# Kernel optimization log

Hardware: AMD Instinct MI355X
Metric: run time of the kernel (lower is better)

Reference implementation:

```python
import jax, jax.numpy as jnp
import numpy as np
from jax import lax

B, L, D, E, K, H = 8, 1024, 256, 8, 2, 1024  # batch, seq(in_channel), in_dim, experts, top_k, out_channel/hidden
LMAX = L // 2  # largest expert input dim (factor i+2 = 2)
LENS = [L // (i + 2) for i in range(E)]


def setup_inputs() -> dict:
    key = jax.random.key(0)
    ks = jax.random.split(key, 12)
    x = jax.random.normal(ks[0], (B, L, D), dtype=jnp.float32)
    conv_ws = jax.random.normal(ks[1], (3, D, D, 3), dtype=jnp.float32) / np.sqrt(3 * D)
    conv_bs = jax.random.normal(ks[2], (3, D), dtype=jnp.float32) * 0.01
    fl_w = jax.random.normal(ks[3], (E, L), dtype=jnp.float32) / np.sqrt(L)
    fl_b = jax.random.normal(ks[4], (E,), dtype=jnp.float32) * 0.01
    # expert first-layer weights, zero-padded on input axis to LMAX (expert i uses L//(i+2) inputs)
    w1 = jax.random.normal(ks[5], (E, H, LMAX), dtype=jnp.float32) / np.sqrt(LMAX)
    col_mask = (np.arange(LMAX)[None, :] < np.array(LENS)[:, None]).astype(np.float32)  # [E, LMAX]
    w1 = w1 * jnp.asarray(col_mask)[:, None, :]
    b1 = jax.random.normal(ks[6], (E, H), dtype=jnp.float32) * 0.01
    w2 = jax.random.normal(ks[7], (E, H, H), dtype=jnp.float32) / np.sqrt(H)
    b2 = jax.random.normal(ks[8], (E, H), dtype=jnp.float32) * 0.01
    w3 = jax.random.normal(ks[9], (E, H, H), dtype=jnp.float32) / np.sqrt(H)
    b3 = jax.random.normal(ks[10], (E, H), dtype=jnp.float32) * 0.01
    return {"x": x, "conv_ws": conv_ws, "conv_bs": conv_bs, "fl_w": fl_w, "fl_b": fl_b,
            "w1": w1, "b1": b1, "w2": w2, "b2": b2, "w3": w3, "b3": b3}


def _gelu(v):
    return jax.nn.gelu(v, approximate=False)  # torch nn.GELU default is exact erf


def _forward(x, conv_ws, conv_bs, fl_w, fl_b, w1, b1, w2, b2, w3, b3):
    xt = jnp.transpose(x, (0, 2, 1))  # [B, D, L]
    # --- Router: 3 dilated causal-padded ('same') convs + GELU ---
    h = xt
    for i in range(3):
        d = 2 ** i
        h = lax.conv_general_dilated(h, conv_ws[i], window_strides=(1,), padding=[(d, d)],
                                     rhs_dilation=(d,), dimension_numbers=("NCH", "OIH", "NCH"))
        h = _gelu(h + conv_bs[i][None, :, None])
    logits = jax.nn.sigmoid(jnp.einsum("bdl,el->bde", h, fl_w) + fl_b)  # [B, D, E]
    prob = jax.nn.softmax(logits, axis=-1)
    top_val, top_idx = lax.top_k(prob, K)  # [B, D, K]
    top_val = top_val / jnp.sum(top_val, axis=-1, keepdims=True)
    # combine gate per expert: gates[b,d,e] = sum_k top_val * 1[top_idx==e]
    gates = jnp.sum(top_val[..., None] * jax.nn.one_hot(top_idx, E, dtype=top_val.dtype), axis=2)  # [B, D, E]
    # --- Per-expert downsample (avg_pool1d, kernel=stride=i+2), zero-padded to LMAX ---
    xs = []
    for i in range(E):
        f = i + 2
        Li = LENS[i]
        xd = xt[:, :, :Li * f].reshape(B, D, Li, f).mean(-1)  # [B, D, Li]
        xs.append(jnp.pad(xd, ((0, 0), (0, 0), (0, LMAX - Li))))
    xe = jnp.stack(xs)  # [E, B, D, LMAX]; pad cols align with zeroed w1 cols
    # --- Expert MLPs (dense compute, masked by gates; zero gate == token not routed) ---
    h1 = _gelu(jnp.einsum("ebdl,ehl->ebdh", xe, w1) + b1[:, None, None, :])
    h2 = _gelu(jnp.einsum("ebdh,egh->ebdg", h1, w2) + b2[:, None, None, :])
    h3 = jnp.einsum("ebdg,eog->ebdo", h2, w3) + b3[:, None, None, :]  # [E, B, D, H]
    out = jnp.einsum("ebdo,bde->bdo", h3, gates)  # scatter-add combine, [B, D, H]
    return jnp.transpose(out, (0, 2, 1))  # [B, L(out_channel), D]


def reference(x, conv_ws, conv_bs, fl_w, fl_b, w1, b1, w2, b2, w3, b3):
    return _forward(x, conv_ws, conv_bs, fl_w, fl_b, w1, b1, w2, b2, w3, b3)
```

## Files before the change

kernel.cpp:

```cpp
#include <hip/hip_runtime.h>
#include <math.h>

#define Bb 8
#define Ll 1024
#define Dd 256
#define Ee 8
#define Hh 1024
#define LMAXc 512
#define NTOK (Bb*Dd)
#define LPAD 1032
#define MAXTILES 72

typedef short bf16x8 __attribute__((ext_vector_type(8)));
typedef float f32x4 __attribute__((ext_vector_type(4)));
typedef unsigned short u16x8 __attribute__((ext_vector_type(8)));

__device__ __forceinline__ float gelu_f(float x) {
    return 0.5f * x * (1.0f + erff(x * 0.70710678118654752440f));
}
__device__ __forceinline__ unsigned short f2b(float x) {
    unsigned int u = __float_as_uint(x);
    return (unsigned short)((u + 0x7fffu + ((u >> 16) & 1u)) >> 16);
}
__device__ __forceinline__ float b2f(unsigned short h) {
    return __uint_as_float(((unsigned int)h) << 16);
}
__device__ __forceinline__ void gl_lds16(const void* g, void* l) {
    __builtin_amdgcn_global_load_lds((const __attribute__((address_space(1))) unsigned int*)g,
                                     (__attribute__((address_space(3))) unsigned int*)l, 16, 0, 0);
}

__global__ __launch_bounds__(256) void prep_all(
    const float* __restrict__ x, const float* __restrict__ cw,
    unsigned short* __restrict__ xhi, unsigned short* __restrict__ xlo,
    unsigned short* __restrict__ chi, unsigned short* __restrict__ clo,
    unsigned short* __restrict__ wchi, unsigned short* __restrict__ wclo,
    unsigned short* __restrict__ xe)
{
    int blk = blockIdx.x;
    int t = threadIdx.x;
    if (blk < 4096) {
        int u = blk;
        int e = u >> 9;
        int b = (u >> 6) & 7;
        int c = u & 63;
        int f = e + 2;
        int Li = Ll / f;
        int j0 = c * 8;
        if (j0 >= Li) return;
        int d = t;
        float invf = 1.0f / (float)f;
        int lim = Li - 1;
        float v[8] = {};
        for (int r = 0; r < f; ++r) {
            #pragma unroll
            for (int jj = 0; jj < 8; ++jj) {
                int j = j0 + jj; if (j > lim) j = lim;
                v[jj] += x[((size_t)(b * Ll + j * f + r)) * Dd + d];
            }
        }
        size_t obase = ((size_t)(e * NTOK + b * 256 + d)) * LMAXc + j0;
        if (j0 + 8 <= Li) {
            u16x8 hv;
            #pragma unroll
            for (int q = 0; q < 8; ++q) hv[q] = (short)f2b(v[q] * invf);
            *(u16x8*)(xe + obase) = hv;
        } else {
            for (int jj = 0; jj < Li - j0; ++jj)
                xe[obase + jj] = f2b(v[jj] * invf);
        }
    } else if (blk < 4128) {
        int u = (blk - 4096) * 256 + t;
        int f = u >> 11;
        int rem = u & 2047;
        int b = rem >> 8;
        int r2 = rem & 255;
        int row = r2 >> 5;
        int col = (r2 & 31) * 8;
        int padrow = (row < 4) ? row : (1024 + row);
        unsigned short* buf = (f == 0) ? xhi : (f == 1) ? xlo : (f == 2) ? chi : clo;
        u16x8 z = {0, 0, 0, 0, 0, 0, 0, 0};
        *(u16x8*)(buf + (size_t)(b * LPAD + padrow) * Dd + col) = z;
    } else if (blk < 4384) {
        int cb = blk - 4128;
        const float4* s4 = (const float4*)x;
        size_t ob = (size_t)cb * 1024 + t;
        float4 v[8];
        #pragma unroll
        for (int it = 0; it < 4; ++it) {
            v[2 * it]     = s4[(ob + it * 256) * 2];
            v[2 * it + 1] = s4[(ob + it * 256) * 2 + 1];
        }
        #pragma unroll
        for (int it = 0; it < 4; ++it) {
            size_t o = ob + it * 256;
            int d8 = (int)(o & 31), l = (int)((o >> 5) & 1023), b = (int)(o >> 15);
            size_t ooff = (size_t)(b * LPAD + 4 + l) * Dd + d8 * 8;
            float vv[8] = {v[2*it].x, v[2*it].y, v[2*it].z, v[2*it].w,
                           v[2*it+1].x, v[2*it+1].y, v[2*it+1].z, v[2*it+1].w};
            u16x8 hv, lv;
            #pragma unroll
            for (int q = 0; q < 8; ++q) {
                unsigned short h = f2b(vv[q]);
                hv[q] = (short)h;
                lv[q] = (short)f2b(vv[q] - b2f(h));
            }
            *(u16x8*)(xhi + ooff) = hv;
            *(u16x8*)(xlo + ooff) = lv;
        }
    } else {
        int cb = blk - 4384;
        int idx0 = (cb * 256 + t) * 8;
        float vv[8];
        #pragma unroll
        for (int q = 0; q < 8; ++q) {
            int idx = idx0 + q;
            int i = idx & (Dd - 1);
            int o = (idx >> 8) & (Dd - 1);
            int lk = idx >> 16;
            int layer = lk / 3;
            int k = lk % 3;
            vv[q] = cw[(((size_t)layer * Dd + o) * Dd + i) * 3 + k];
        }
        u16x8 hv, lv;
        #pragma unroll
        for (int q = 0; q < 8; ++q) {
            unsigned short h = f2b(vv[q]);
            hv[q] = (short)h;
            lv[q] = (short)f2b(vv[q] - b2f(h));
        }
        *(u16x8*)(wchi + idx0) = hv;
        *(u16x8*)(wclo + idx0) = lv;
    }
}

template<int MODE, int CVT>
__global__ __launch_bounds__(256, 2) void conv_mfma(
    const unsigned short* __restrict__ inhi, const unsigned short* __restrict__ inlo,
    const unsigned short* __restrict__ whiL, const unsigned short* __restrict__ wloL,
    const float* __restrict__ bias,
    unsigned short* __restrict__ outhi, unsigned short* __restrict__ outlo,
    const float* __restrict__ flw, float* __restrict__ logits,
    const float* __restrict__ cvsrc, unsigned short* __restrict__ cvd1,
    unsigned short* __restrict__ cvd2, int dil)
{
    __shared__ char smem[32768];

    if (CVT && blockIdx.y >= (Dd / 64)) {
        int cb = (blockIdx.y - Dd / 64) * 128 + blockIdx.x;
        int t = threadIdx.x;
        const float4* s4 = (const float4*)cvsrc;
        size_t ob = (size_t)cb * 1024 + t;
        float4 v[8];
        #pragma unroll
        for (int it = 0; it < 4; ++it) {
            v[2 * it]     = s4[(ob + it * 256) * 2];
            v[2 * it + 1] = s4[(ob + it * 256) * 2 + 1];
        }
        #pragma unroll
        for (int it = 0; it < 4; ++it) {
            size_t o = ob + it * 256;
            float vv[8] = {v[2*it].x, v[2*it].y, v[2*it].z, v[2*it].w,
                           v[2*it+1].x, v[2*it+1].y, v[2*it+1].z, v[2*it+1].w};
            u16x8 hv, lv;
            #pragma unroll
            for (int q = 0; q < 8; ++q) {
                unsigned short h = f2b(vv[q]);
                hv[q] = (short)h;
                if (CVT == 1) lv[q] = (short)f2b(vv[q] - b2f(h));
            }
            *(u16x8*)(cvd1 + o * 8) = hv;
            if (CVT == 1) *(u16x8*)(cvd2 + o * 8) = lv;
        }
        return;
    }

    char* sAhi = smem;
    char* sAlo = smem + 8192;
    char* sBhi = smem + 16384;
    char* sBlo = smem + 24576;

    const int t = threadIdx.x;
    const int lane = t & 63, w = t >> 6;
    const int r16 = lane & 15, quad = lane >> 4;
    const int wr = w >> 1, wc = w & 1;
    const int row0 = blockIdx.x * 64;
    const int col0 = blockIdx.y * 64;
    const int b = row0 >> 10, l0 = row0 & 1023;

    int aoff[2], boff[2];
    #pragma unroll
    for (int i = 0; i < 2; ++i) {
        int ra = wr * 32 + i * 16 + r16;
        aoff[i] = ra * 64 + ((quad ^ ((ra >> 1) & 3)) << 4);
        int rb = wc * 32 + i * 16 + r16;
        boff[i] = rb * 64 + ((quad ^ ((rb >> 1) & 3)) << 4);
    }
    const int rs = t >> 2, ce = ((t & 3) ^ ((rs >> 1) & 3)) << 3;
    const unsigned short* gAhi = inhi + (size_t)(b * LPAD + 4 + l0 + rs) * Dd + ce;
    const unsigned short* gAlo = inlo + (size_t)(b * LPAD + 4 + l0 + rs) * Dd + ce;

    f32x4 acc[2][2];
    const f32x4 zero4 = {0.f, 0.f, 0.f, 0.f};
    #pragma unroll
    for (int i = 0; i < 2; ++i)
        #pragma unroll
        for (int j = 0; j < 2; ++j) acc[i][j] = zero4;

    for (int tap = 0; tap < 3; ++tap) {
        const int sh = (tap - 1) * dil;
        const unsigned short* pAhi = gAhi + sh * Dd;
        const unsigned short* pAlo = gAlo + sh * Dd;
        const unsigned short* gBhi = whiL + ((size_t)tap * Dd + col0 + rs) * Dd + ce;
        const unsigned short* gBlo = wloL + ((size_t)tap * Dd + col0 + rs) * Dd + ce;
        for (int kb = 0; kb < Dd; kb += 64) {
            gl_lds16(pAhi + kb,      sAhi + (w << 10));
            gl_lds16(pAhi + kb + 32, sAhi + 4096 + (w << 10));
            gl_lds16(pAlo + kb,      sAlo + (w << 10));
            gl_lds16(pAlo + kb + 32, sAlo + 4096 + (w << 10));
            gl_lds16(gBhi + kb,      sBhi + (w << 10));
            gl_lds16(gBhi + kb + 32, sBhi + 4096 + (w << 10));
            gl_lds16(gBlo + kb,      sBlo + (w << 10));
            gl_lds16(gBlo + kb + 32, sBlo + 4096 + (w << 10));
            __syncthreads();
            #pragma unroll
            for (int h = 0; h < 2; ++h) {
                const int ho = h * 4096;
                bf16x8 ah[2], al[2], bh[2], bl[2];
                #pragma unroll
                for (int i = 0; i < 2; ++i) {
                    ah[i] = *(const bf16x8*)(sAhi + ho + aoff[i]);
                    al[i] = *(const bf16x8*)(sAlo + ho + aoff[i]);
                    bh[i] = *(const bf16x8*)(sBhi + ho + boff[i]);
                    bl[i] = *(const bf16x8*)(sBlo + ho + boff[i]);
                }
                #pragma unroll
                for (int mi = 0; mi < 2; ++mi)
                    #pragma unroll
                    for (int ni = 0; ni < 2; ++ni) {
                        acc[mi][ni] = __builtin_amdgcn_mfma_f32_16x16x32_bf16(ah[mi], bh[ni], acc[mi][ni], 0, 0, 0);
                        acc[mi][ni] = __builtin_amdgcn_mfma_f32_16x16x32_bf16(ah[mi], bl[ni], acc[mi][ni], 0, 0, 0);
                        acc[mi][ni] = __builtin_amdgcn_mfma_f32_16x16x32_bf16(al[mi], bh[ni], acc[mi][ni], 0, 0, 0);
                    }
            }
            __syncthreads();
        }
    }

    int cc[2]; float bv[2];
    #pragma unroll
    for (int ni = 0; ni < 2; ++ni) {
        cc[ni] = col0 + wc * 32 + ni * 16 + r16;
        bv[ni] = bias[cc[ni]];
    }
    if (MODE == 0) {
        #pragma unroll
        for (int mi = 0; mi < 2; ++mi) {
            int lb = l0 + wr * 32 + mi * 16 + quad * 4;
            #pragma unroll
            for (int reg = 0; reg < 4; ++reg) {
                int l = lb + reg;
                #pragma unroll
                for (int ni = 0; ni < 2; ++ni) {
                    float v = gelu_f(acc[mi][ni][reg] + bv[ni]);
                    size_t o = (size_t)(b * LPAD + 4 + l) * Dd + cc[ni];
                    unsigned short h = f2b(v);
                    outhi[o] = h;
                    outlo[o] = f2b(v - b2f(h));
                }
            }
        }
    } else {
        float* wl   = (float*)smem;
        float* slog = (float*)(smem + 2048);
        for (int i = t; i < 512; i += 256) {
            int ll = i >> 3, e = i & 7;
            wl[i] = flw[e * Ll + l0 + ll];
            slog[i] = 0.0f;
        }
        __syncthreads();
        float part[2][8];
        #pragma unroll
        for (int ni = 0; ni < 2; ++ni)
            #pragma unroll
            for (int e = 0; e < 8; ++e) part[ni][e] = 0.0f;
        #pragma unroll
        for (int mi = 0; mi < 2; ++mi) {
            #pragma unroll
            for (int reg = 0; reg < 4; ++reg) {
                int ll = wr * 32 + mi * 16 + quad * 4 + reg;
                #pragma unroll
                for (int ni = 0; ni < 2; ++ni) {
                    float v = gelu_f(acc[mi][ni][reg] + bv[ni]);
                    #pragma unroll
                    for (int e = 0; e < 8; ++e) part[ni][e] += v * wl[ll * 8 + e];
                }
            }
        }
        #pragma unroll
        for (int ni = 0; ni < 2; ++ni) {
            int dl = wc * 32 + ni * 16 + r16;
            #pragma unroll
            for (int e = 0; e < 8; ++e) atomicAdd(&slog[dl * 8 + e], part[ni][e]);
        }
        __syncthreads();
        for (int i = t; i < 512; i += 256) {
            int dl = i >> 3, e = i & 7;
            atomicAdd(&logits[(size_t)(b * Dd + col0 + dl) * Ee + e], slog[i]);
        }
    }
}

template<int MODE, int GATHER, int TWOPASS>
__global__ __launch_bounds__(256, 4) void gemm_sp(
    const unsigned short* __restrict__ AG,
    const unsigned short* __restrict__ BhiG, const unsigned short* __restrict__ BloG,
    const float* __restrict__ biasG, const float* __restrict__ gates,
    const int* __restrict__ cntG, const int* __restrict__ listG,
    const int* __restrict__ tileTab, const int* __restrict__ ntiles,
    unsigned short* __restrict__ Cout, float* __restrict__ outf,
    int M, int N, int K)
{
    if (blockIdx.y >= ntiles[0]) return;
    const int desc = tileTab[blockIdx.y];
    const int e = desc >> 16;
    const int row0 = (desc & 0xffff) * 64;
    const int cn = cntG[e];

    constexpr int NCH = TWOPASS ? 2 : 4;
    __shared__ char smem[TWOPASS ? 24576 : 32768];
    char* sA   = smem;
    char* sBhi = smem + NCH * 4096;
    char* sBlo = smem + 2 * NCH * 4096;

    const unsigned short* Bhi = BhiG + (size_t)e * N * K;
    const unsigned short* Blo = TWOPASS ? (BloG + (size_t)e * N * K) : nullptr;
    const float* bias = biasG + (size_t)e * N;

    int Keff = K;
    if (GATHER) {
        int Li = Ll / (e + 2);
        Keff = ((Li + 63) >> 6) << 6;
    }

    const int t = threadIdx.x;
    const int lane = t & 63, w = t >> 6;
    const int r16 = lane & 15, quad = lane >> 4;
    const int wr = w >> 1, wc = w & 1;
    const int col0 = blockIdx.x * 64;

    int aoff[2], boff[2];
    #pragma unroll
    for (int i = 0; i < 2; ++i) {
        int ra = wr * 32 + i * 16 + r16;
        aoff[i] = ra * 64 + ((quad ^ ((ra >> 1) & 3)) << 4);
        int rb = wc * 32 + i * 16 + r16;
        boff[i] = rb * 64 + ((quad ^ ((rb >> 1) & 3)) << 4);
    }
    const int r0s = t >> 2, c0s = ((t & 3) ^ ((r0s >> 1) & 3)) << 3;
    int ri = row0 + r0s; if (ri > cn - 1) ri = cn - 1;
    const int ar = GATHER ? listG[e * NTOK + ri] : ri;
    const unsigned short* gA  = AG + ((size_t)e * M + ar) * K + c0s;
    const unsigned short* gB  = Bhi + (size_t)(col0 + r0s) * K + c0s;
    const unsigned short* gBl = TWOPASS ? (Blo + (size_t)(col0 + r0s) * K + c0s) : nullptr;
    const int wofs = w << 10;

    f32x4 acc[2][2];
    const f32x4 zero4 = {0.f, 0.f, 0.f, 0.f};
    #pragma unroll
    for (int i = 0; i < 2; ++i)
        #pragma unroll
        for (int j = 0; j < 2; ++j) acc[i][j] = zero4;

    for (int k0 = 0; k0 < Keff; k0 += NCH * 32) {
        #pragma unroll
        for (int c = 0; c < NCH; ++c) {
            gl_lds16(gA + k0 + c * 32, sA + c * 4096 + wofs);
            gl_lds16(gB + k0 + c * 32, sBhi + c * 4096 + wofs);
        }
        if (TWOPASS) {
            #pragma unroll
            for (int c = 0; c < NCH; ++c)
                gl_lds16(gBl + k0 + c * 32, sBlo + c * 4096 + wofs);
        }
        __syncthreads();
        #pragma unroll
        for (int h = 0; h < NCH; ++h) {
            const int ho = h * 4096;
            bf16x8 ah[2], bh[2];
            #pragma unroll
            for (int i = 0; i < 2; ++i) {
                ah[i] = *(const bf16x8*)(sA + ho + aoff[i]);
                bh[i] = *(const bf16x8*)(sBhi + ho + boff[i]);
            }
            #pragma unroll
            for (int mi = 0; mi < 2; ++mi)
                #pragma unroll
                for (int ni = 0; ni < 2; ++ni)
                    acc[mi][ni] = __builtin_amdgcn_mfma_f32_16x16x32_bf16(ah[mi], bh[ni], acc[mi][ni], 0, 0, 0);
            if (TWOPASS) {
                bf16x8 bl[2];
                #pragma unroll
                for (int i = 0; i < 2; ++i) bl[i] = *(const bf16x8*)(sBlo + ho + boff[i]);
                #pragma unroll
                for (int mi = 0; mi < 2; ++mi)
                    #pragma unroll
                    for (int ni = 0; ni < 2; ++ni)
                        acc[mi][ni] = __builtin_amdgcn_mfma_f32_16x16x32_bf16(ah[mi], bl[ni], acc[mi][ni], 0, 0, 0);
            }
        }
        __syncthreads();
    }

    int cc[2]; float bv[2];
    #pragma unroll
    for (int ni = 0; ni < 2; ++ni) {
        cc[ni] = col0 + wc * 32 + ni * 16 + r16;
        bv[ni] = bias[cc[ni]];
    }
    if (MODE == 0) {
        unsigned short* CE = Cout + (size_t)e * M * N;
        #pragma unroll
        for (int mi = 0; mi < 2; ++mi) {
            int rb = row0 + wr * 32 + mi * 16 + quad * 4;
            #pragma unroll
            for (int reg = 0; reg < 4; ++reg) {
                size_t roff = (size_t)(rb + reg) * N;
                #pragma unroll
                for (int ni = 0; ni < 2; ++ni)
                    CE[roff + cc[ni]] = f2b(gelu_f(acc[mi][ni][reg] + bv[ni]));
            }
        }
    } else {
        #pragma unroll
        for (int mi = 0; mi < 2; ++mi) {
            int rb = row0 + wr * 32 + mi * 16 + quad * 4;
            #pragma unroll
            for (int reg = 0; reg < 4; ++reg) {
                int i = rb + reg;
                if (i < cn) {
                    int tok = listG[e * NTOK + i];
                    float g = gates[(size_t)tok * Ee + e];
                    size_t roff = ((size_t)e * NTOK + i) * N;
                    #pragma unroll
                    for (int ni = 0; ni < 2; ++ni)
                        outf[roff + cc[ni]] = g * (acc[mi][ni][reg] + bv[ni]);
                }
            }
        }
    }
}


__global__ __launch_bounds__(256) void gates_topk(const float* __restrict__ logits,
                                                  const float* __restrict__ fl_b,
                                                  float* __restrict__ gates,
                                                  int* __restrict__ cnt,
                                                  int* __restrict__ list,
                                                  int* __restrict__ rowidx) {
    const int tok = blockIdx.x * 256 + threadIdx.x;
    const int lane = threadIdx.x & 63;
    const unsigned long long ltmask = (1ull << lane) - 1ull;

    float s[Ee];
    #pragma unroll
    for (int e = 0; e < Ee; ++e) {
        float z = logits[tok * Ee + e] + fl_b[e];
        s[e] = 1.0f / (1.0f + expf(-z));
    }
    float mx = s[0];
    #pragma unroll
    for (int e = 1; e < Ee; ++e) mx = fmaxf(mx, s[e]);
    float p[Ee];
    #pragma unroll
    for (int e = 0; e < Ee; ++e) p[e] = expf(s[e] - mx);
    int i1 = 0;
    #pragma unroll
    for (int e = 1; e < Ee; ++e) if (p[e] > p[i1]) i1 = e;
    int i2 = (i1 == 0) ? 1 : 0;
    #pragma unroll
    for (int e = 0; e < Ee; ++e) {
        if (e == i1 || e == i2) continue;
        if (p[e] > p[i2]) i2 = e;
    }
    float inv = 1.0f / (p[i1] + p[i2]);
    #pragma unroll
    for (int e = 0; e < Ee; ++e) gates[tok * Ee + e] = 0.0f;
    gates[tok * Ee + i1] = p[i1] * inv;
    gates[tok * Ee + i2] = p[i2] * inv;

    #pragma unroll
    for (int slot = 0; slot < 2; ++slot) {
        int ie = slot ? i2 : i1;
        for (int e = 0; e < Ee; ++e) {
            unsigned long long m = __ballot(ie == e);
            if (m) {
                int leader = __ffsll((long long)m) - 1;
                int base = 0;
                if (lane == leader) base = atomicAdd(&cnt[e], (int)__popcll(m));
                base = __shfl(base, leader);
                if (ie == e) {
                    int pos = base + (int)__popcll(m & ltmask);
                    list[e * NTOK + pos] = tok;
                    rowidx[tok * 2 + slot] = e * NTOK + pos;
                }
            }
        }
    }
}

__global__ void tiletab_build(const int* __restrict__ cnt,
                              int* __restrict__ tileTab,
                              int* __restrict__ ntiles) {
    if (threadIdx.x == 0) {
        int nt = 0;
        for (int e = 0; e < Ee; ++e) {
            int c = cnt[e];
            for (int m = 0; m * 64 < c; ++m) tileTab[nt++] = (e << 16) | m;
        }
        ntiles[0] = nt;
    }
}

__global__ __launch_bounds__(256) void combine_out(const float* __restrict__ h3g,
                                                   const int* __restrict__ rowidx,
                                                   float* __restrict__ out) {
    __shared__ float tile[32][33];
    int b = blockIdx.z;
    int d0 = blockIdx.x * 32;
    int o0 = blockIdx.y * 32;
    int tx = threadIdx.x & 31, ty = threadIdx.x >> 5;
    for (int i = 0; i < 32; i += 8) {
        int tok = b * Dd + d0 + ty + i;
        int r0 = rowidx[tok * 2];
        int r1 = rowidx[tok * 2 + 1];
        tile[ty + i][tx] = h3g[(size_t)r0 * Hh + o0 + tx] + h3g[(size_t)r1 * Hh + o0 + tx];
    }
    __syncthreads();
    for (int i = 0; i < 32; i += 8)
        out[((size_t)b * Hh + o0 + ty + i) * Dd + d0 + tx] = tile[tx][ty + i];
}

extern "C" void kernel_launch(void* const* d_in, const int* in_sizes, int n_in,
                              void* d_out, int out_size, void* d_ws, size_t ws_size,
                              hipStream_t stream) {
    const float* x       = (const float*)d_in[0];
    const float* conv_w  = (const float*)d_in[1];
    const float* conv_b  = (const float*)d_in[2];
    const float* fl_w    = (const float*)d_in[3];
    const float* fl_b    = (const float*)d_in[4];
    const float* w1      = (const float*)d_in[5];
    const float* b1      = (const float*)d_in[6];
    const float* w2      = (const float*)d_in[7];
    const float* b2      = (const float*)d_in[8];
    const float* w3      = (const float*)d_in[9];
    const float* b3      = (const float*)d_in[10];
    float* out = (float*)d_out;

    char* ws = (char*)d_ws;
    unsigned short* xphi = (unsigned short*)(ws);
    unsigned short* xplo = (unsigned short*)(ws + 4227072);
    unsigned short* cphi = (unsigned short*)(ws + 8454144);
    unsigned short* cplo = (unsigned short*)(ws + 12681216);
    unsigned short* wchi = (unsigned short*)(ws + 16908288);
    unsigned short* wclo = (unsigned short*)(ws + 18087936);
    unsigned short* h1   = (unsigned short*)(ws);
    unsigned short* h2   = (unsigned short*)(ws + 67108864);
    float*          h3g  = (float*)(ws);
    unsigned short* xe   = (unsigned short*)(ws + 67108864);
    unsigned short* w1hi = (unsigned short*)(ws + 83886080);
    unsigned short* w1lo = (unsigned short*)(ws + 92274688);
    unsigned short* w2b  = (unsigned short*)(ws + 100663296);
    unsigned short* w3b  = (unsigned short*)(ws + 117440512);
    float* logits  = (float*)(ws + 134217728);
    int*   cnt     = (int*)(ws + 134283264);
    int*   ntiles  = (int*)(ws + 134283296);
    int*   tileTab = (int*)(ws + 134283328);
    float* gates   = (float*)(ws + 134284288);
    int*   list    = (int*)(ws + 134349824);
    int*   rowidx  = (int*)(ws + 134415360);

    hipMemsetAsync(logits, 0, 65536 + 64, stream);

    prep_all<<<4672, 256, 0, stream>>>(x, conv_w, xphi, xplo, cphi, cplo,
                                       wchi, wclo, xe);

    const int WL = 3 * Dd * Dd;
    conv_mfma<0, 1><<<dim3(Bb * Ll / 64, Dd / 64 + 4), 256, 0, stream>>>(
        xphi, xplo, wchi + 0 * WL, wclo + 0 * WL, conv_b + 0 * Dd, cphi, cplo,
        nullptr, nullptr, w1, w1hi, w1lo, 1);
    conv_mfma<0, 2><<<dim3(Bb * Ll / 64, Dd / 64 + 8), 256, 0, stream>>>(
        cphi, cplo, wchi + 1 * WL, wclo + 1 * WL, conv_b + 1 * Dd, xphi, xplo,
        nullptr, nullptr, w2, w2b, nullptr, 2);
    conv_mfma<1, 2><<<dim3(Bb * Ll / 64, Dd / 64 + 8), 256, 0, stream>>>(
        xphi, xplo, wchi + 2 * WL, wclo + 2 * WL, conv_b + 2 * Dd, nullptr, nullptr,
        fl_w, logits, w3, w3b, nullptr, 4);

    gates_topk<<<NTOK / 256, 256, 0, stream>>>(logits, fl_b, gates, cnt, list, rowidx);
    tiletab_build<<<1, 64, 0, stream>>>(cnt, tileTab, ntiles);

    gemm_sp<0, 1, 1><<<dim3(16, MAXTILES), 256, 0, stream>>>(
        xe, w1hi, w1lo, b1, nullptr, cnt, list, tileTab, ntiles, h1, nullptr, NTOK, Hh, LMAXc);

    gemm_sp<0, 0, 0><<<dim3(16, MAXTILES), 256, 0, stream>>>(
        h1, w2b, nullptr, b2, nullptr, cnt, list, tileTab, ntiles, h2, nullptr, NTOK, Hh, Hh);

    gemm_sp<1, 0, 0><<<dim3(16, MAXTILES), 256, 0, stream>>>(
        h2, w3b, nullptr, b3, gates, cnt, list, tileTab, ntiles, nullptr, h3g, NTOK, Hh, Hh);

    combine_out<<<dim3(Dd / 32, Hh / 32, Bb), 256, 0, stream>>>(h3g, rowidx, out);
}
```

Before: 293.4 us.

## Enlarge conv MFMA row tile to 128 and compute expert tiles inline

The router conv kernel now covers 128 sequence rows per block instead of 64, with each wave computing four 16-row fragments. This doubles reuse of each loaded weight tile and halves the block count, at the cost of more LDS (48KB) and more accumulator registers, which may lower occupancy. The conversion side-blocks are re-indexed to match the new grid shape. Separately, the single-thread tiletab_build launch is removed and each gemm_sp block finds its expert and tile by scanning the per-expert counts, saving one kernel launch.

```diff
diff --git a/kernel.cpp b/kernel.cpp
--- a/kernel.cpp
+++ b/kernel.cpp
@@ -144,10 +144,10 @@
     const float* __restrict__ cvsrc, unsigned short* __restrict__ cvd1,
     unsigned short* __restrict__ cvd2, int dil)
 {
-    __shared__ char smem[32768];
+    __shared__ char smem[49152];
 
     if (CVT && blockIdx.y >= (Dd / 64)) {
-        int cb = (blockIdx.y - Dd / 64) * 128 + blockIdx.x;
+        int cb = (blockIdx.y - Dd / 64) * 64 + blockIdx.x;
         int t = threadIdx.x;
         const float4* s4 = (const float4*)cvsrc;
         size_t ob = (size_t)cb * 1024 + t;
@@ -176,66 +176,78 @@
     }
 
     char* sAhi = smem;
-    char* sAlo = smem + 8192;
-    char* sBhi = smem + 16384;
-    char* sBlo = smem + 24576;
+    char* sAlo = smem + 16384;
+    char* sBhi = smem + 32768;
+    char* sBlo = smem + 40960;
 
     const int t = threadIdx.x;
     const int lane = t & 63, w = t >> 6;
     const int r16 = lane & 15, quad = lane >> 4;
     const int wr = w >> 1, wc = w & 1;
-    const int row0 = blockIdx.x * 64;
+    const int row0 = blockIdx.x * 128;
     const int col0 = blockIdx.y * 64;
     const int b = row0 >> 10, l0 = row0 & 1023;
 
-    int aoff[2], boff[2];
+    int aoff[4], boff[2];
+    #pragma unroll
+    for (int i = 0; i < 4; ++i) {
+        int ra = wr * 64 + i * 16 + r16;
+        aoff[i] = ra * 64 + ((quad ^ ((ra >> 1) & 3)) << 4);
+    }
     #pragma unroll
     for (int i = 0; i < 2; ++i) {
-        int ra = wr * 32 + i * 16 + r16;
-        aoff[i] = ra * 64 + ((quad ^ ((ra >> 1) & 3)) << 4);
         int rb = wc * 32 + i * 16 + r16;
         boff[i] = rb * 64 + ((quad ^ ((rb >> 1) & 3)) << 4);
     }
     const int rs = t >> 2, ce = ((t & 3) ^ ((rs >> 1) & 3)) << 3;
-    const unsigned short* gAhi = inhi + (size_t)(b * LPAD + 4 + l0 + rs) * Dd + ce;
-    const unsigned short* gAlo = inlo + (size_t)(b * LPAD + 4 + l0 + rs) * Dd + ce;
-
-    f32x4 acc[2][2];
+    const unsigned short* gAhi0 = inhi + (size_t)(b * LPAD + 4 + l0 + rs) * Dd + ce;
+    const unsigned short* gAhi1 = gAhi0 + 64 * Dd;
+    const unsigned short* gAlo0 = inlo + (size_t)(b * LPAD + 4 + l0 + rs) * Dd + ce;
+    const unsigned short* gAlo1 = gAlo0 + 64 * Dd;
+
+    f32x4 acc[4][2];
     const f32x4 zero4 = {0.f, 0.f, 0.f, 0.f};
     #pragma unroll
-    for (int i = 0; i < 2; ++i)
+    for (int i = 0; i < 4; ++i)
         #pragma unroll
         for (int j = 0; j < 2; ++j) acc[i][j] = zero4;
 
     for (int tap = 0; tap < 3; ++tap) {
         const int sh = (tap - 1) * dil;
-        const unsigned short* pAhi = gAhi + sh * Dd;
-        const unsigned short* pAlo = gAlo + sh * Dd;
+        const unsigned short* pAhi0 = gAhi0 + sh * Dd;
+        const unsigned short* pAhi1 = gAhi1 + sh * Dd;
+        const unsigned short* pAlo0 = gAlo0 + sh * Dd;
+        const unsigned short* pAlo1 = gAlo1 + sh * Dd;
         const unsigned short* gBhi = whiL + ((size_t)tap * Dd + col0 + rs) * Dd + ce;
         const unsigned short* gBlo = wloL + ((size_t)tap * Dd + col0 + rs) * Dd + ce;
         for (int kb = 0; kb < Dd; kb += 64) {
-            gl_lds16(pAhi + kb,      sAhi + (w << 10));
-            gl_lds16(pAhi + kb + 32, sAhi + 4096 + (w << 10));
-            gl_lds16(pAlo + kb,      sAlo + (w << 10));
-            gl_lds16(pAlo + kb + 32, sAlo + 4096 + (w << 10));
-            gl_lds16(gBhi + kb,      sBhi + (w << 10));
-            gl_lds16(gBhi + kb + 32, sBhi + 4096 + (w << 10));
-            gl_lds16(gBlo + kb,      sBlo + (w << 10));
-            gl_lds16(gBlo + kb + 32, sBlo + 4096 + (w << 10));
+            #pragma unroll
+            for (int c = 0; c < 2; ++c) {
+                int kc = kb + c * 32;
+                gl_lds16(pAhi0 + kc, sAhi + c * 8192 + (w << 10));
+                gl_lds16(pAhi1 + kc, sAhi + c * 8192 + 4096 + (w << 10));
+                gl_lds16(pAlo0 + kc, sAlo + c * 8192 + (w << 10));
+                gl_lds16(pAlo1 + kc, sAlo + c * 8192 + 4096 + (w << 10));
+                gl_lds16(gBhi + kc,  sBhi + c * 4096 + (w << 10));
+                gl_lds16(gBlo + kc,  sBlo + c * 4096 + (w << 10));
+            }
             __syncthreads();
             #pragma unroll
             for (int h = 0; h < 2; ++h) {
-                const int ho = h * 4096;
-                bf16x8 ah[2], al[2], bh[2], bl[2];
+                const int hoA = h * 8192, hoB = h * 4096;
+                bf16x8 ah[4], al[4], bh[2], bl[2];
+                #pragma unroll
+                for (int i = 0; i < 4; ++i) {
+                    ah[i] = *(const bf16x8*)(sAhi + hoA + aoff[i]);
+                    al[i] = *(const bf16x8*)(sAlo + hoA + aoff[i]);
+                }
                 #pragma unroll
                 for (int i = 0; i < 2; ++i) {
-                    ah[i] = *(const bf16x8*)(sAhi + ho + aoff[i]);
-                    al[i] = *(const bf16x8*)(sAlo + ho + aoff[i]);
-                    bh[i] = *(const bf16x8*)(sBhi + ho + boff[i]);
-                    bl[i] = *(const bf16x8*)(sBlo + ho + boff[i]);
+                    bh[i] = *(const bf16x8*)(sBhi + hoB + boff[i]);
+                    bl[i] = *(const bf16x8*)(sBlo + hoB + boff[i]);
                 }
                 #pragma unroll
-                for (int mi = 0; mi < 2; ++mi)
+                for (int mi = 0; mi < 4; ++mi)
                     #pragma unroll
                     for (int ni = 0; ni < 2; ++ni) {
                         acc[mi][ni] = __builtin_amdgcn_mfma_f32_16x16x32_bf16(ah[mi], bh[ni], acc[mi][ni], 0, 0, 0);
@@ -255,8 +267,8 @@
     }
     if (MODE == 0) {
         #pragma unroll
-        for (int mi = 0; mi < 2; ++mi) {
-            int lb = l0 + wr * 32 + mi * 16 + quad * 4;
+        for (int mi = 0; mi < 4; ++mi) {
+            int lb = l0 + wr * 64 + mi * 16 + quad * 4;
             #pragma unroll
             for (int reg = 0; reg < 4; ++reg) {
                 int l = lb + reg;
@@ -272,12 +284,12 @@
         }
     } else {
         float* wl   = (float*)smem;
-        float* slog = (float*)(smem + 2048);
-        for (int i = t; i < 512; i += 256) {
+        float* slog = (float*)(smem + 4096);
+        for (int i = t; i < 1024; i += 256) {
             int ll = i >> 3, e = i & 7;
             wl[i] = flw[e * Ll + l0 + ll];
-            slog[i] = 0.0f;
-        }
+        }
+        for (int i = t; i < 512; i += 256) slog[i] = 0.0f;
         __syncthreads();
         float part[2][8];
         #pragma unroll
@@ -285,10 +297,10 @@
             #pragma unroll
             for (int e = 0; e < 8; ++e) part[ni][e] = 0.0f;
         #pragma unroll
-        for (int mi = 0; mi < 2; ++mi) {
+        for (int mi = 0; mi < 4; ++mi) {
             #pragma unroll
             for (int reg = 0; reg < 4; ++reg) {
-                int ll = wr * 32 + mi * 16 + quad * 4 + reg;
+                int ll = wr * 64 + mi * 16 + quad * 4 + reg;
                 #pragma unroll
                 for (int ni = 0; ni < 2; ++ni) {
                     float v = gelu_f(acc[mi][ni][reg] + bv[ni]);
@@ -317,14 +329,18 @@
     const unsigned short* __restrict__ BhiG, const unsigned short* __restrict__ BloG,
     const float* __restrict__ biasG, const float* __restrict__ gates,
     const int* __restrict__ cntG, const int* __restrict__ listG,
-    const int* __restrict__ tileTab, const int* __restrict__ ntiles,
     unsigned short* __restrict__ Cout, float* __restrict__ outf,
     int M, int N, int K)
 {
-    if (blockIdx.y >= ntiles[0]) return;
-    const int desc = tileTab[blockIdx.y];
-    const int e = desc >> 16;
-    const int row0 = (desc & 0xffff) * 64;
+    int m = blockIdx.y, e;
+    #pragma unroll
+    for (e = 0; e < Ee; ++e) {
+        int te = (cntG[e] + 63) >> 6;
+        if (m < te) break;
+        m -= te;
+    }
+    if (e == Ee) return;
+    const int row0 = m * 64;
     const int cn = cntG[e];
 
     constexpr int NCH = TWOPASS ? 2 : 4;
@@ -506,19 +522,6 @@
                 }
             }
         }
-    }
-}
-
-__global__ void tiletab_build(const int* __restrict__ cnt,
-                              int* __restrict__ tileTab,
-                              int* __restrict__ ntiles) {
-    if (threadIdx.x == 0) {
-        int nt = 0;
-        for (int e = 0; e < Ee; ++e) {
-            int c = cnt[e];
-            for (int m = 0; m * 64 < c; ++m) tileTab[nt++] = (e << 16) | m;
-        }
-        ntiles[0] = nt;
     }
 }
 
@@ -574,8 +577,6 @@
     unsigned short* w3b  = (unsigned short*)(ws + 117440512);
     float* logits  = (float*)(ws + 134217728);
     int*   cnt     = (int*)(ws + 134283264);
-    int*   ntiles  = (int*)(ws + 134283296);
-    int*   tileTab = (int*)(ws + 134283328);
     float* gates   = (float*)(ws + 134284288);
     int*   list    = (int*)(ws + 134349824);
     int*   rowidx  = (int*)(ws + 134415360);
@@ -586,27 +587,26 @@
                                        wchi, wclo, xe);
 
     const int WL = 3 * Dd * Dd;
-    conv_mfma<0, 1><<<dim3(Bb * Ll / 64, Dd / 64 + 4), 256, 0, stream>>>(
+    conv_mfma<0, 1><<<dim3(Bb * Ll / 128, Dd / 64 + 8), 256, 0, stream>>>(
         xphi, xplo, wchi + 0 * WL, wclo + 0 * WL, conv_b + 0 * Dd, cphi, cplo,
         nullptr, nullptr, w1, w1hi, w1lo, 1);
-    conv_mfma<0, 2><<<dim3(Bb * Ll / 64, Dd / 64 + 8), 256, 0, stream>>>(
+    conv_mfma<0, 2><<<dim3(Bb * Ll / 128, Dd / 64 + 16), 256, 0, stream>>>(
         cphi, cplo, wchi + 1 * WL, wclo + 1 * WL, conv_b + 1 * Dd, xphi, xplo,
         nullptr, nullptr, w2, w2b, nullptr, 2);
-    conv_mfma<1, 2><<<dim3(Bb * Ll / 64, Dd / 64 + 8), 256, 0, stream>>>(
+    conv_mfma<1, 2><<<dim3(Bb * Ll / 128, Dd / 64 + 16), 256, 0, stream>>>(
         xphi, xplo, wchi + 2 * WL, wclo + 2 * WL, conv_b + 2 * Dd, nullptr, nullptr,
         fl_w, logits, w3, w3b, nullptr, 4);
 
     gates_topk<<<NTOK / 256, 256, 0, stream>>>(logits, fl_b, gates, cnt, list, rowidx);
-    tiletab_build<<<1, 64, 0, stream>>>(cnt, tileTab, ntiles);
 
     gemm_sp<0, 1, 1><<<dim3(16, MAXTILES), 256, 0, stream>>>(
-        xe, w1hi, w1lo, b1, nullptr, cnt, list, tileTab, ntiles, h1, nullptr, NTOK, Hh, LMAXc);
+        xe, w1hi, w1lo, b1, nullptr, cnt, list, h1, nullptr, NTOK, Hh, LMAXc);
 
     gemm_sp<0, 0, 0><<<dim3(16, MAXTILES), 256, 0, stream>>>(
-        h1, w2b, nullptr, b2, nullptr, cnt, list, tileTab, ntiles, h2, nullptr, NTOK, Hh, Hh);
+        h1, w2b, nullptr, b2, nullptr, cnt, list, h2, nullptr, NTOK, Hh, Hh);
 
     gemm_sp<1, 0, 0><<<dim3(16, MAXTILES), 256, 0, stream>>>(
-        h2, w3b, nullptr, b3, gates, cnt, list, tileTab, ntiles, nullptr, h3g, NTOK, Hh, Hh);
+        h2, w3b, nullptr, b3, gates, cnt, list, nullptr, h3g, NTOK, Hh, Hh);
 
     combine_out<<<dim3(Dd / 32, Hh / 32, Bb), 256, 0, stream>>>(h3g, rowidx, out);
 }
```

Result: slower. 310.5 us (+5.8%).
